# Kernel optimization log

Measured on AMD Instinct MI355X. Metric: run time of the kernel, lower is better.

The kernel has to match this reference:

```python
import jax, jax.numpy as jnp
import numpy as np
from jax import lax

# Static problem sizes (see shape_source): 128 events x 512 points each
G, P, K = 128, 512, 16          # graphs, points per graph, knn k
FEAT = 128                       # n_samples*2
PLANES = [128, 96, 64, 32]       # linear reduction, n_graph=3, graph_out=32
N_OUT = 3                        # n_type


def setup_inputs() -> dict:
    key = jax.random.key(0)
    ks = jax.random.split(key, 24)
    N = G * P
    x = jax.random.normal(ks[0], (N, FEAT), jnp.float32)
    # coo: integer detector coords (cols 0,1) + graph id (col 2)
    xy = jax.random.randint(ks[1], (N, 2), 0, 32).astype(jnp.int32)
    gid = jnp.repeat(jnp.arange(G, dtype=jnp.int32), P)
    coo = jnp.concatenate([xy, gid[:, None]], axis=1)  # [N,3]
    inp = {"x": x, "coo": coo}
    # SAGEConv params per layer: lin_l (neighbor-mean path, with bias), lin_r (root path)
    ki = 2
    for l, (nin, nout) in enumerate(zip(PLANES[:-1], PLANES[1:])):
        s = 1.0 / np.sqrt(nin)
        inp[f"wl{l}"] = jax.random.normal(ks[ki], (nin, nout), jnp.float32) * s; ki += 1
        inp[f"wr{l}"] = jax.random.normal(ks[ki], (nin, nout), jnp.float32) * s; ki += 1
        inp[f"b{l}"] = jnp.zeros((nout,), jnp.float32)
    # MLP head: 32 -> 32 -> 3 with ReLU between (n_lin = 2)
    inp["lw0"] = jax.random.normal(ks[ki], (PLANES[-1], PLANES[-1]), jnp.float32) / np.sqrt(PLANES[-1]); ki += 1
    inp["lb0"] = jnp.zeros((PLANES[-1],), jnp.float32)
    inp["lw1"] = jax.random.normal(ks[ki], (PLANES[-1], N_OUT), jnp.float32) / np.sqrt(PLANES[-1]); ki += 1
    inp["lb1"] = jnp.zeros((N_OUT,), jnp.float32)
    return inp


def _knn_indices(coo):
    # knn_graph(coo, k, batch=coo[:,2], loop=False): k nearest within each graph,
    # self excluded. Batch segments are uniform size P so reshape per-graph.
    pos = coo.reshape(G, P, 3).astype(jnp.float32)
    d2 = jnp.sum((pos[:, :, None, :] - pos[:, None, :, :]) ** 2, axis=-1)  # [G,P,P]
    d2 = jnp.where(jnp.eye(P, dtype=bool), jnp.inf, d2)  # loop=False
    _, idx = lax.top_k(-d2, K)  # [G,P,K] neighbor (source) indices per target
    return idx


def reference(x, coo, wl0, wr0, b0, wl1, wr1, b1, wl2, wr2, b2, lw0, lb0, lw1, lb1):
    idx = _knn_indices(coo)
    h = x.reshape(G, P, FEAT)
    gather = jax.vmap(lambda hg, ig: hg[ig])  # per-graph neighbor gather
    for wl, wr, b in ((wl0, wr0, b0), (wl1, wr1, b1), (wl2, wr2, b2)):
        nbr_mean = gather(h, idx).mean(axis=2)  # [G,P,K,nin] -> [G,P,nin]
        # SAGEConv: lin_l(mean_j x_j) + lin_r(x_i), then ReLU (GraphLayer)
        h = jax.nn.relu(jnp.einsum('gpi,io->gpo', nbr_mean, wl)
                        + jnp.einsum('gpi,io->gpo', h, wr) + b)
    pooled = h.max(axis=1)  # global_max_pool over batch -> [G, 32]
    hid = jax.nn.relu(pooled @ lw0 + lb0)
    return hid @ lw1 + lb1  # [G, 3]
```

## Files before the change

kernel.cpp:

```cpp
#include <hip/hip_runtime.h>

#define G 128
#define P 512
#define K 16
#define NPTS (G * P)

typedef _Float16 half8 __attribute__((ext_vector_type(8)));
typedef float    floatx4 __attribute__((ext_vector_type(4)));

__device__ __forceinline__ unsigned uminu(unsigned a, unsigned b) { return a < b ? a : b; }

__device__ __forceinline__ void ce(unsigned& a, unsigned& b) {
    const unsigned lo = a < b ? a : b;
    const unsigned hi = a < b ? b : a;
    a = lo; b = hi;
}

__device__ __forceinline__ void sort16(unsigned k[16]) {
#pragma unroll
    for (int p = 1; p < 16; p <<= 1) {
#pragma unroll
        for (int q = p; q >= 1; q >>= 1) {
#pragma unroll
            for (int j = q % p; j + q < 16; j += 2 * q) {
#pragma unroll
                for (int i = 0; i < q; ++i) {
                    const int a = i + j, b2 = i + j + q;
                    if (b2 < 16 && (a / (2 * p)) == (b2 / (2 * p)))
                        ce(k[a], k[b2]);
                }
            }
        }
    }
}

__device__ __forceinline__ void halfmerge(unsigned best[16], const unsigned kb[16]) {
#pragma unroll
    for (int i = 0; i < 16; ++i) best[i] = uminu(best[i], kb[15 - i]);
#pragma unroll
    for (int d = 8; d >= 1; d >>= 1)
#pragma unroll
        for (int i = 0; i < 16; ++i)
            if ((i & d) == 0) ce(best[i], best[i + d]);
}

template <int KT, int NIN, int NOUT>
__device__ __forceinline__ void prep_elem(int e, const float* __restrict__ wl,
                                          const float* __restrict__ wr,
                                          _Float16* __restrict__ wf) {
    const int fr   = e >> 9;
    const int lane = (e >> 3) & 63;
    const int j    = e & 7;
    const int ntile = fr / KT;
    const int kt    = fr - ntile * KT;
    const int k = kt * 32 + ((lane >> 4) << 3) + j;
    const int n = ntile * 16 + (lane & 15);
    const float v = (k < NIN) ? wl[k * NOUT + n] : wr[(k - NIN) * NOUT + n];
    wf[e] = (_Float16)v;
}

__global__ __launch_bounds__(512, 4)
void pre_kernel(const int* __restrict__ coo, int* __restrict__ idx_out,
                const float* __restrict__ x, _Float16* __restrict__ x16,
                const float* __restrict__ wl0, const float* __restrict__ wr0,
                const float* __restrict__ wl1, const float* __restrict__ wr1,
                const float* __restrict__ wl2, const float* __restrict__ wr2,
                _Float16* __restrict__ wf0, _Float16* __restrict__ wf1,
                _Float16* __restrict__ wf2) {
    __shared__ float2 sxy[P];
    __shared__ unsigned mk[7][64][17];
    const int b   = blockIdx.x;
    const int tid = threadIdx.x;

    if (b < 1024) {
        const int g   = b >> 3;
        const int t0  = (b & 7) * 64;
        const int tgt = tid & 63;
        const int sub = tid >> 6;

        for (int i = tid; i < P; i += 512) {
            const int* cp = coo + (size_t)(g * P + i) * 3;
            sxy[i] = make_float2((float)cp[0], (float)cp[1]);
        }
        __syncthreads();

        const int tg = t0 + tgt;
        const float px = sxy[tg].x, py = sxy[tg].y;

        unsigned best[K];
#pragma unroll
        for (int k = 0; k < K; ++k) best[k] = 0xFFFFFFF0u + k;

        const int s0 = sub * 64;
#pragma unroll
        for (int batch = 0; batch < 4; ++batch) {
            unsigned kb[K];
#pragma unroll
            for (int j = 0; j < 16; ++j) {
                const int s = s0 + batch * 16 + j;
                const float2 c = sxy[s];
                const float dx = px - c.x, dy = py - c.y;
                const float keyf = fmaf(fmaf(dx, dx, dy * dy), 512.f, (float)s);
                unsigned key = (unsigned)keyf;
                if (s == tg) key = 0xFFFFFFFFu;
                kb[j] = key;
            }
            sort16(kb);
            halfmerge(best, kb);
        }

        if (sub != 0) {
#pragma unroll
            for (int k = 0; k < K; ++k) mk[sub - 1][tgt][k] = best[k];
        }
        __syncthreads();
        if (sub == 0) {
#pragma unroll 1
            for (int ss = 0; ss < 7; ++ss) {
                unsigned pb[K];
#pragma unroll
                for (int k = 0; k < K; ++k) pb[k] = mk[ss][tgt][k];
                halfmerge(best, pb);
            }
            int4* op = (int4*)(idx_out + (size_t)(g * P + tg) * K);
#pragma unroll
            for (int q4 = 0; q4 < 4; ++q4) {
                int4 o;
                o.x = (int)(best[q4 * 4 + 0] & (unsigned)(P - 1));
                o.y = (int)(best[q4 * 4 + 1] & (unsigned)(P - 1));
                o.z = (int)(best[q4 * 4 + 2] & (unsigned)(P - 1));
                o.w = (int)(best[q4 * 4 + 3] & (unsigned)(P - 1));
                op[q4] = o;
            }
        }
    } else if (b < 3072) {
        const int i = (b - 1024) * 512 + tid;
        const float4* p = (const float4*)(x + (size_t)i * 8);
        const float4 a = p[0], bq = p[1];
        half8 o;
        o[0] = (_Float16)a.x;  o[1] = (_Float16)a.y;
        o[2] = (_Float16)a.z;  o[3] = (_Float16)a.w;
        o[4] = (_Float16)bq.x; o[5] = (_Float16)bq.y;
        o[6] = (_Float16)bq.z; o[7] = (_Float16)bq.w;
        *(half8*)(x16 + (size_t)i * 8) = o;
    } else {
        const int e = (b - 3072) * 512 + tid;
        if (e < 24576)      prep_elem<8, 128, 96>(e,         wl0, wr0, wf0);
        else if (e < 36864) prep_elem<6,  96, 64>(e - 24576, wl1, wr1, wf1);
        else                prep_elem<4,  64, 32>(e - 36864, wl2, wr2, wf2);
    }
}

template <int CIN, int NOUT, bool FOUT16>
__global__ __launch_bounds__(256, 4)
void sage_kernel(const _Float16* __restrict__ hin, const int* __restrict__ idxg,
                 const _Float16* __restrict__ wf, const float* __restrict__ bias,
                 void* __restrict__ hout) {
    constexpr int KTm = CIN / 32;
    constexpr int KT  = CIN / 16;
    constexpr int NH  = NOUT / 32;
    constexpr int RS  = 136;

    __shared__ _Float16 As[64 * RS];

    const int tid  = threadIdx.x;
    const int b    = blockIdx.x;
    const int slot = b >> 3;
    const int g    = (b & 7) | ((slot & 15) << 3);
    const int n0   = g * P + (slot >> 4) * 64;
    const _Float16* __restrict__ hg = hin + (size_t)(g * P) * CIN;

    const int pt = tid >> 2;
    const int q  = tid & 3;

    const int4* ip = (const int4*)(idxg + (size_t)(n0 + pt) * K);
    const int4 na = ip[0], nb4 = ip[1], nc = ip[2], nd = ip[3];
    const int nn[16] = {na.x, na.y, na.z, na.w, nb4.x, nb4.y, nb4.z, nb4.w,
                        nc.x, nc.y, nc.z, nc.w, nd.x, nd.y, nd.z, nd.w};

#pragma unroll 1
    for (int c = 0; c < KTm; ++c) {
        const int ch = c * 32 + q * 8;
        half8 a0 = {}; half8 a1 = {};
#pragma unroll
        for (int k = 0; k < 16; k += 4) {
            const half8 v0 = *(const half8*)(hg + (size_t)nn[k + 0] * CIN + ch);
            const half8 v1 = *(const half8*)(hg + (size_t)nn[k + 1] * CIN + ch);
            const half8 v2 = *(const half8*)(hg + (size_t)nn[k + 2] * CIN + ch);
            const half8 v3 = *(const half8*)(hg + (size_t)nn[k + 3] * CIN + ch);
            a0 += v0; a1 += v1; a0 += v2; a1 += v3;
        }
        half8 m;
#pragma unroll
        for (int e = 0; e < 8; ++e)
            m[e] = (_Float16)(((float)a0[e] + (float)a1[e]) * 0.0625f);
        *(half8*)&As[pt * RS + (c * 4 + q) * 8] = m;
    }

    const int l  = tid & 63;
    const int wv = tid >> 6;
    const int mh = wv & 1;
    const int nh = wv >> 1;
    const int lm = l & 15, lq = l >> 4;

    float bs[NH];
#pragma unroll
    for (int nt = 0; nt < NH; ++nt)
        bs[nt] = bias[nh * (NOUT / 2) + nt * 16 + lm];

    __syncthreads();

    floatx4 acc[2][NH];
#pragma unroll
    for (int mt = 0; mt < 2; ++mt)
#pragma unroll
        for (int nt = 0; nt < NH; ++nt) {
            floatx4 z = {0.f, 0.f, 0.f, 0.f};
            acc[mt][nt] = z;
        }

#pragma unroll
    for (int kt = 0; kt < KT; ++kt) {
        half8 bfr[NH];
#pragma unroll
        for (int nt = 0; nt < NH; ++nt) {
            const int ng = nh * NH + nt;
            bfr[nt] = *(const half8*)(wf + ((size_t)(ng * KT + kt) * 64 + l) * 8);
        }
#pragma unroll
        for (int mt = 0; mt < 2; ++mt) {
            const int row = mh * 32 + mt * 16 + lm;
            half8 a;
            if (kt < KTm) {
                a = *(const half8*)&As[row * RS + (kt * 4 + lq) * 8];
            } else {
                a = *(const half8*)(hin + (size_t)(n0 + row) * CIN +
                                    (kt - KTm) * 32 + lq * 8);
            }
#pragma unroll
            for (int nt = 0; nt < NH; ++nt)
                acc[mt][nt] = __builtin_amdgcn_mfma_f32_16x16x32_f16(
                    a, bfr[nt], acc[mt][nt], 0, 0, 0);
        }
    }

#pragma unroll
    for (int mt = 0; mt < 2; ++mt)
#pragma unroll
        for (int nt = 0; nt < NH; ++nt) {
            const int n = nh * (NOUT / 2) + nt * 16 + lm;
#pragma unroll
            for (int r = 0; r < 4; ++r) {
                const int p = n0 + mh * 32 + mt * 16 + lq * 4 + r;
                float v = acc[mt][nt][r] + bs[nt];
                v = v > 0.f ? v : 0.f;
                if constexpr (FOUT16)
                    ((_Float16*)hout)[(size_t)p * NOUT + n] = (_Float16)v;
                else
                    ((float*)hout)[(size_t)p * NOUT + n] = v;
            }
        }
}

__global__ __launch_bounds__(256)
void head_kernel(const _Float16* __restrict__ h3, const float* __restrict__ lw0,
                 const float* __restrict__ lb0, const float* __restrict__ lw1,
                 const float* __restrict__ lb1, float* __restrict__ out) {
    __shared__ float red[256];
    __shared__ float pooled[32];
    __shared__ float hid[32];
    const int g = blockIdx.x;
    const int t = threadIdx.x;
    const int c = t & 31;
    const int r = t >> 5;

    const _Float16* hb = h3 + (size_t)g * P * 32;
    float m = -3.4e38f;
    for (int p = r; p < P; p += 8) m = fmaxf(m, (float)hb[p * 32 + c]);
    red[t] = m;
    __syncthreads();
    if (r < 4) red[t] = fmaxf(red[t], red[t + 128]);
    __syncthreads();
    if (r < 2) red[t] = fmaxf(red[t], red[t + 64]);
    __syncthreads();
    if (r == 0) pooled[c] = fmaxf(red[t], red[t + 32]);
    __syncthreads();

    if (t < 32) {
        float a = lb0[t];
#pragma unroll
        for (int i = 0; i < 32; ++i) a += pooled[i] * lw0[i * 32 + t];
        hid[t] = a > 0.f ? a : 0.f;
    }
    __syncthreads();
    if (t < 3) {
        float a = lb1[t];
#pragma unroll
        for (int i = 0; i < 32; ++i) a += hid[i] * lw1[i * 3 + t];
        out[g * 3 + t] = a;
    }
}

extern "C" void kernel_launch(void* const* d_in, const int* in_sizes, int n_in,
                              void* d_out, int out_size, void* d_ws, size_t ws_size,
                              hipStream_t stream) {
    const float* x   = (const float*)d_in[0];
    const int*   coo = (const int*)  d_in[1];
    const float* wl0 = (const float*)d_in[2];
    const float* wr0 = (const float*)d_in[3];
    const float* b0  = (const float*)d_in[4];
    const float* wl1 = (const float*)d_in[5];
    const float* wr1 = (const float*)d_in[6];
    const float* b1  = (const float*)d_in[7];
    const float* wl2 = (const float*)d_in[8];
    const float* wr2 = (const float*)d_in[9];
    const float* b2  = (const float*)d_in[10];
    const float* lw0 = (const float*)d_in[11];
    const float* lb0 = (const float*)d_in[12];
    const float* lw1 = (const float*)d_in[13];
    const float* lb1 = (const float*)d_in[14];
    float* out = (float*)d_out;

    char* ws = (char*)d_ws;
    _Float16* wf0 = (_Float16*)(ws + 0);
    _Float16* wf1 = (_Float16*)(ws + 49152);
    _Float16* wf2 = (_Float16*)(ws + 73728);
    int*      idx = (int*)     (ws + 81920);
    _Float16* x16 = (_Float16*)(ws + 4276224);
    _Float16* h1  = (_Float16*)(ws + 21053440);
    _Float16* h2  = (_Float16*)(ws + 33636352);
    _Float16* h3  = (_Float16*)(ws + 42024960);

    pre_kernel<<<3152, 512, 0, stream>>>(coo, idx, x, x16,
                                         wl0, wr0, wl1, wr1, wl2, wr2,
                                         wf0, wf1, wf2);

    sage_kernel<128, 96, true><<<NPTS / 64, 256, 0, stream>>>(x16, idx, wf0, b0, h1);
    sage_kernel< 96, 64, true><<<NPTS / 64, 256, 0, stream>>>(h1,  idx, wf1, b1, h2);
    sage_kernel< 64, 32, true><<<NPTS / 64, 256, 0, stream>>>(h2,  idx, wf2, b2, h3);

    head_kernel<<<G, 256, 0, stream>>>(h3, lw0, lb0, lw1, lb1, out);
}
```

Baseline: 172.6 us.

## Fuse three SAGE layers and head into one persistent kernel with grid barriers

Replaces the three sage_kernel launches and head_kernel with a single 1024-block kernel that runs each layer in turn, separated by atomic-counter grid barriers. The last layer max-pools per 64-point chunk in registers and shared memory instead of writing h3, and the head reduces these partial maxima. This removes launch gaps and the h3 round trip through global memory. The cost is a memset, spin-wait barriers, and reliance on all 1024 blocks being co-resident (4 per CU across 256 CUs), which risks deadlock if occupancy falls short.

```diff
diff --git a/kernel.cpp b/kernel.cpp
--- a/kernel.cpp
+++ b/kernel.cpp
@@ -151,23 +151,34 @@
     }
 }
 
-template <int CIN, int NOUT, bool FOUT16>
-__global__ __launch_bounds__(256, 4)
-void sage_kernel(const _Float16* __restrict__ hin, const int* __restrict__ idxg,
-                 const _Float16* __restrict__ wf, const float* __restrict__ bias,
-                 void* __restrict__ hout) {
+__device__ __forceinline__ void gridbar(unsigned* ctr) {
+    __syncthreads();
+    if (threadIdx.x == 0) {
+        __hip_atomic_fetch_add(ctr, 1u, __ATOMIC_ACQ_REL, __HIP_MEMORY_SCOPE_AGENT);
+        unsigned v;
+        do {
+            __builtin_amdgcn_s_sleep(2);
+            v = __hip_atomic_load(ctr, __ATOMIC_ACQUIRE, __HIP_MEMORY_SCOPE_AGENT);
+        } while (v < 1024u);
+    }
+    __syncthreads();
+}
+
+template <int CIN, int NOUT, bool POOL>
+__device__ __forceinline__ void sage_body(
+    const int b, const int tid, _Float16* __restrict__ As, float (*ps)[16],
+    const _Float16* __restrict__ hin, const int* __restrict__ idxg,
+    const _Float16* __restrict__ wf, const float* __restrict__ bias,
+    _Float16* __restrict__ hout, float* __restrict__ pool_part) {
     constexpr int KTm = CIN / 32;
     constexpr int KT  = CIN / 16;
     constexpr int NH  = NOUT / 32;
     constexpr int RS  = 136;
 
-    __shared__ _Float16 As[64 * RS];
-
-    const int tid  = threadIdx.x;
-    const int b    = blockIdx.x;
     const int slot = b >> 3;
     const int g    = (b & 7) | ((slot & 15) << 3);
-    const int n0   = g * P + (slot >> 4) * 64;
+    const int chunk = slot >> 4;
+    const int n0   = g * P + chunk * 64;
     const _Float16* __restrict__ hg = hin + (size_t)(g * P) * CIN;
 
     const int pt = tid >> 2;
@@ -244,60 +255,90 @@
         }
     }
 
-#pragma unroll
-    for (int mt = 0; mt < 2; ++mt)
-#pragma unroll
-        for (int nt = 0; nt < NH; ++nt) {
-            const int n = nh * (NOUT / 2) + nt * 16 + lm;
+    if constexpr (POOL) {
+        float vmax = -3.4e38f;
+#pragma unroll
+        for (int mt = 0; mt < 2; ++mt)
 #pragma unroll
             for (int r = 0; r < 4; ++r) {
-                const int p = n0 + mh * 32 + mt * 16 + lq * 4 + r;
-                float v = acc[mt][nt][r] + bs[nt];
+                float v = acc[mt][0][r] + bs[0];
                 v = v > 0.f ? v : 0.f;
-                if constexpr (FOUT16)
-                    ((_Float16*)hout)[(size_t)p * NOUT + n] = (_Float16)v;
-                else
-                    ((float*)hout)[(size_t)p * NOUT + n] = v;
-            }
-        }
-}
-
-__global__ __launch_bounds__(256)
-void head_kernel(const _Float16* __restrict__ h3, const float* __restrict__ lw0,
-                 const float* __restrict__ lb0, const float* __restrict__ lw1,
-                 const float* __restrict__ lb1, float* __restrict__ out) {
-    __shared__ float red[256];
+                vmax = fmaxf(vmax, v);
+            }
+        vmax = fmaxf(vmax, __shfl_xor(vmax, 16, 64));
+        vmax = fmaxf(vmax, __shfl_xor(vmax, 32, 64));
+        if (lq == 0) ps[wv][lm] = vmax;
+        __syncthreads();
+        if (tid < 32) {
+            const int nh2 = tid >> 4, lm2 = tid & 15;
+            const float m = fmaxf(ps[nh2 * 2][lm2], ps[nh2 * 2 + 1][lm2]);
+            pool_part[(size_t)(g * 8 + chunk) * 32 + tid] = m;
+        }
+    } else {
+#pragma unroll
+        for (int mt = 0; mt < 2; ++mt)
+#pragma unroll
+            for (int nt = 0; nt < NH; ++nt) {
+                const int n = nh * (NOUT / 2) + nt * 16 + lm;
+#pragma unroll
+                for (int r = 0; r < 4; ++r) {
+                    const int p = n0 + mh * 32 + mt * 16 + lq * 4 + r;
+                    float v = acc[mt][nt][r] + bs[nt];
+                    v = v > 0.f ? v : 0.f;
+                    hout[(size_t)p * NOUT + n] = (_Float16)v;
+                }
+            }
+    }
+}
+
+__global__ __launch_bounds__(256, 4)
+void gnn_kernel(const _Float16* __restrict__ x16, const int* __restrict__ idx,
+                const _Float16* __restrict__ wf0, const float* __restrict__ b0,
+                const _Float16* __restrict__ wf1, const float* __restrict__ b1,
+                const _Float16* __restrict__ wf2, const float* __restrict__ b2,
+                _Float16* __restrict__ h1, _Float16* __restrict__ h2,
+                float* __restrict__ pool_part,
+                const float* __restrict__ lw0, const float* __restrict__ lb0,
+                const float* __restrict__ lw1, const float* __restrict__ lb1,
+                float* __restrict__ out, unsigned* __restrict__ ctr) {
+    __shared__ _Float16 As[64 * 136];
+    __shared__ float ps[4][16];
     __shared__ float pooled[32];
     __shared__ float hid[32];
-    const int g = blockIdx.x;
-    const int t = threadIdx.x;
-    const int c = t & 31;
-    const int r = t >> 5;
-
-    const _Float16* hb = h3 + (size_t)g * P * 32;
-    float m = -3.4e38f;
-    for (int p = r; p < P; p += 8) m = fmaxf(m, (float)hb[p * 32 + c]);
-    red[t] = m;
-    __syncthreads();
-    if (r < 4) red[t] = fmaxf(red[t], red[t + 128]);
-    __syncthreads();
-    if (r < 2) red[t] = fmaxf(red[t], red[t + 64]);
-    __syncthreads();
-    if (r == 0) pooled[c] = fmaxf(red[t], red[t + 32]);
-    __syncthreads();
-
-    if (t < 32) {
-        float a = lb0[t];
-#pragma unroll
-        for (int i = 0; i < 32; ++i) a += pooled[i] * lw0[i * 32 + t];
-        hid[t] = a > 0.f ? a : 0.f;
-    }
-    __syncthreads();
-    if (t < 3) {
-        float a = lb1[t];
-#pragma unroll
-        for (int i = 0; i < 32; ++i) a += hid[i] * lw1[i * 3 + t];
-        out[g * 3 + t] = a;
+
+    const int b   = blockIdx.x;
+    const int tid = threadIdx.x;
+
+    sage_body<128, 96, false>(b, tid, As, ps, x16, idx, wf0, b0, h1, nullptr);
+    gridbar(ctr + 0);
+    sage_body< 96, 64, false>(b, tid, As, ps, h1, idx, wf1, b1, h2, nullptr);
+    gridbar(ctr + 16);
+    sage_body< 64, 32, true >(b, tid, As, ps, h2, idx, wf2, b2, nullptr, pool_part);
+    gridbar(ctr + 32);
+
+    if (b < 128) {
+        const int g = b;
+        if (tid < 32) {
+            float m = pool_part[(size_t)(g * 8) * 32 + tid];
+#pragma unroll
+            for (int c = 1; c < 8; ++c)
+                m = fmaxf(m, pool_part[(size_t)(g * 8 + c) * 32 + tid]);
+            pooled[tid] = m;
+        }
+        __syncthreads();
+        if (tid < 32) {
+            float a = lb0[tid];
+#pragma unroll
+            for (int i = 0; i < 32; ++i) a += pooled[i] * lw0[i * 32 + tid];
+            hid[tid] = a > 0.f ? a : 0.f;
+        }
+        __syncthreads();
+        if (tid < 3) {
+            float a = lb1[tid];
+#pragma unroll
+            for (int i = 0; i < 32; ++i) a += hid[i] * lw1[i * 3 + tid];
+            out[g * 3 + tid] = a;
+        }
     }
 }
 
@@ -329,15 +370,16 @@
     _Float16* x16 = (_Float16*)(ws + 4276224);
     _Float16* h1  = (_Float16*)(ws + 21053440);
     _Float16* h2  = (_Float16*)(ws + 33636352);
-    _Float16* h3  = (_Float16*)(ws + 42024960);
+    float*    pool= (float*)   (ws + 42024960);
+    unsigned* ctr = (unsigned*)(ws + 42156032);
+
+    hipMemsetAsync(ctr, 0, 192, stream);
 
     pre_kernel<<<3152, 512, 0, stream>>>(coo, idx, x, x16,
                                          wl0, wr0, wl1, wr1, wl2, wr2,
                                          wf0, wf1, wf2);
 
-    sage_kernel<128, 96, true><<<NPTS / 64, 256, 0, stream>>>(x16, idx, wf0, b0, h1);
-    sage_kernel< 96, 64, true><<<NPTS / 64, 256, 0, stream>>>(h1,  idx, wf1, b1, h2);
-    sage_kernel< 64, 32, true><<<NPTS / 64, 256, 0, stream>>>(h2,  idx, wf2, b2, h3);
-
-    head_kernel<<<G, 256, 0, stream>>>(h3, lw0, lb0, lw1, lb1, out);
-}
+    gnn_kernel<<<1024, 256, 0, stream>>>(x16, idx, wf0, b0, wf1, b1, wf2, b2,
+                                         h1, h2, pool, lw0, lb0, lw1, lb1,
+                                         out, ctr);
+}
```

After: 665.4 us. 3.86x slower.
